# Kernel optimization log

Hardware: AMD Instinct MI355X
Metric: run time of the kernel (lower is better)

The kernel has to match this reference:

```python
import jax, jax.numpy as jnp
import numpy as np

def setup_inputs() -> dict:
    key = jax.random.key(0)
    k1, k2 = jax.random.split(key)
    bb_feats = jax.random.normal(k1, (8, 512, 128, 128), dtype=jnp.float32)
    aux_out = jax.random.normal(k2, (8, 19, 128, 128), dtype=jnp.float32)
    return {"bb_feats": bb_feats, "aux_out": aux_out}

def reference(bb_feats, aux_out):
    B, K, H, W = aux_out.shape
    C = bb_feats.shape[1]
    probs = jax.nn.softmax(aux_out.reshape(B, K, H * W), axis=2)  # [B,K,HW]
    feats = bb_feats.reshape(B, C, H * W)                          # [B,C,HW]
    # weighted sum over spatial dim: [B,K,HW] x [B,C,HW] -> [B,K,C]
    ctx = jnp.einsum('bks,bcs->bkc', probs, feats)
    # -> [B,C,K,1]
    return jnp.transpose(ctx, (0, 2, 1))[..., None]
```

## Files before the change

kernel.cpp:

```cpp
#include <hip/hip_runtime.h>
#include <math.h>

#define B 8
#define C 512
#define K 19
#define HW 16384
#define ROWS (B * K)
#define L2E 1.44269504088896340736f

#define NW 4
#define CPW 4
#define CPB (CPW * NW)
#define CG (C / CPB)
#define NSC 4
#define SCHUNK (HW / NSC)
#define TS 256
#define NT (SCHUNK / TS)

__global__ __launch_bounds__(1024)
void probs_kernel(const float* __restrict__ aux, float* __restrict__ probs,
                  float* __restrict__ out) {
    int row  = blockIdx.x;
    int tid  = threadIdx.x;
    int lane = tid & 63;
    int wave = tid >> 6;
    __shared__ float red[16];

    if (row < 19)
        ((float4*)out)[(size_t)row * 1024 + tid] = make_float4(0.f, 0.f, 0.f, 0.f);

    const float4* x4 = (const float4*)(aux + (size_t)row * HW);
    float4*       p4 = (float4*)(probs + (size_t)row * HW);

    float4 v[4];
    #pragma unroll
    for (int i = 0; i < 4; i++) v[i] = x4[tid + i * 1024];

    float m = -INFINITY;
    #pragma unroll
    for (int i = 0; i < 4; i++)
        m = fmaxf(m, fmaxf(fmaxf(v[i].x, v[i].y), fmaxf(v[i].z, v[i].w)));
    #pragma unroll
    for (int off = 32; off > 0; off >>= 1) m = fmaxf(m, __shfl_xor(m, off, 64));
    if (lane == 0) red[wave] = m;
    __syncthreads();
    #pragma unroll
    for (int w = 0; w < 16; w++) m = fmaxf(m, red[w]);
    __syncthreads();

    float nm = -m * L2E;
    float s = 0.f;
    #pragma unroll
    for (int i = 0; i < 4; i++) {
        v[i].x = exp2f(fmaf(v[i].x, L2E, nm));
        v[i].y = exp2f(fmaf(v[i].y, L2E, nm));
        v[i].z = exp2f(fmaf(v[i].z, L2E, nm));
        v[i].w = exp2f(fmaf(v[i].w, L2E, nm));
        s += (v[i].x + v[i].y) + (v[i].z + v[i].w);
    }
    #pragma unroll
    for (int off = 32; off > 0; off >>= 1) s += __shfl_xor(s, off, 64);
    if (lane == 0) red[wave] = s;
    __syncthreads();
    float Z = 0.f;
    #pragma unroll
    for (int w = 0; w < 16; w++) Z += red[w];
    float inv = 1.0f / Z;

    #pragma unroll
    for (int i = 0; i < 4; i++) {
        float4 o;
        o.x = v[i].x * inv; o.y = v[i].y * inv;
        o.z = v[i].z * inv; o.w = v[i].w * inv;
        p4[tid + i * 1024] = o;
    }
}

__global__ __launch_bounds__(256)
__attribute__((amdgpu_waves_per_eu(2)))
void gather_kernel(const float* __restrict__ feats, const float* __restrict__ probs,
                   float* __restrict__ out) {
    int bid = blockIdx.x;
    int xcd = bid & 7;
    int lid = xcd * 128 + (bid >> 3);
    int cg  = lid & (CG - 1);
    int grp = lid >> 5;
    int sc  = grp & (NSC - 1);
    int b   = grp >> 2;

    int tid  = threadIdx.x;
    int lane = tid & 63;
    int wave = tid >> 6;
    int c0   = cg * CPB + wave * CPW;

    const float* Pbase = probs + (size_t)b * K * HW + sc * SCHUNK + lane * 4;
    const float* Fbase = feats + ((size_t)b * C + c0) * HW + sc * SCHUNK;

    float acc[CPW][K];
    #pragma unroll
    for (int c = 0; c < CPW; c++)
        #pragma unroll
        for (int k = 0; k < K; k++) acc[c][k] = 0.f;

    float4 f_cur[CPW], f_next[CPW];
    #pragma unroll
    for (int c = 0; c < CPW; c++)
        f_cur[c] = *(const float4*)(Fbase + c * HW + lane * 4);

    for (int t = 0; t < NT; t++) {
        int s = t * TS;
        if (t + 1 < NT) {
            int s1 = s + TS;
            #pragma unroll
            for (int c = 0; c < CPW; c++)
                f_next[c] = *(const float4*)(Fbase + c * HW + s1 + lane * 4);
        }

        float4 p_cur = *(const float4*)(Pbase + s);
        #pragma unroll
        for (int k = 0; k < K; k++) {
            float4 p_nxt;
            if (k + 1 < K)
                p_nxt = *(const float4*)(Pbase + (size_t)(k + 1) * HW + s);
            #pragma unroll
            for (int c = 0; c < CPW; c++) {
                acc[c][k] = fmaf(p_cur.x, f_cur[c].x, acc[c][k]);
                acc[c][k] = fmaf(p_cur.y, f_cur[c].y, acc[c][k]);
                acc[c][k] = fmaf(p_cur.z, f_cur[c].z, acc[c][k]);
                acc[c][k] = fmaf(p_cur.w, f_cur[c].w, acc[c][k]);
            }
            p_cur = p_nxt;
        }

        #pragma unroll
        for (int c = 0; c < CPW; c++) f_cur[c] = f_next[c];
    }

    #pragma unroll
    for (int c = 0; c < CPW; c++)
        #pragma unroll
        for (int k = 0; k < K; k++) {
            float v = acc[c][k];
            #pragma unroll
            for (int off = 32; off > 0; off >>= 1) v += __shfl_xor(v, off, 64);
            if (lane == 0)
                atomicAdd(&out[((size_t)b * C + c0 + c) * K + k], v);
        }
}

extern "C" void kernel_launch(void* const* d_in, const int* in_sizes, int n_in,
                              void* d_out, int out_size, void* d_ws, size_t ws_size,
                              hipStream_t stream) {
    const float* feats = (const float*)d_in[0];
    const float* aux   = (const float*)d_in[1];
    float* out   = (float*)d_out;
    float* probs = (float*)d_ws;

    probs_kernel<<<ROWS, 1024, 0, stream>>>(aux, probs, out);
    gather_kernel<<<B * CG * NSC, 256, 0, stream>>>(feats, probs, out);
}
```

Measured before the change: 434.7 us.

## Stage probs tiles in LDS via async global_load_lds with double buffering

Each block now stages its shared probability tile (19 rows × 256 positions) into a double-buffered LDS array using async global_load_lds, instead of having every wave reload probs from global memory. Feature loads are double-buffered in registers, and manual vmcnt waits plus barriers order the pipeline. A per-block rotation of the tile order spreads concurrent blocks across different memory addresses. This is meant to cut redundant global and L2 traffic for probs and to overlap loads with FMAs, at the cost of block-wide barriers, extra LDS use, and fragile hand-counted waitcnt logic.

Result: faster. 399.8 us (-8.0%).

```diff
diff --git a/kernel.cpp b/kernel.cpp
--- a/kernel.cpp
+++ b/kernel.cpp
@@ -16,6 +16,9 @@
 #define SCHUNK (HW / NSC)
 #define TS 256
 #define NT (SCHUNK / TS)
+
+typedef __attribute__((address_space(3))) unsigned int lds_u32;
+typedef const __attribute__((address_space(1))) unsigned int glb_u32;
 
 __global__ __launch_bounds__(1024)
 void probs_kernel(const float* __restrict__ aux, float* __restrict__ probs,
@@ -80,6 +83,8 @@
 __attribute__((amdgpu_waves_per_eu(2)))
 void gather_kernel(const float* __restrict__ feats, const float* __restrict__ probs,
                    float* __restrict__ out) {
+    __shared__ float plds[2][K][TS];
+
     int bid = blockIdx.x;
     int xcd = bid & 7;
     int lid = xcd * 128 + (bid >> 3);
@@ -87,14 +92,15 @@
     int grp = lid >> 5;
     int sc  = grp & (NSC - 1);
     int b   = grp >> 2;
+    int rot = (bid * 11) & (NT - 1);
 
     int tid  = threadIdx.x;
     int lane = tid & 63;
     int wave = tid >> 6;
     int c0   = cg * CPB + wave * CPW;
 
-    const float* Pbase = probs + (size_t)b * K * HW + sc * SCHUNK + lane * 4;
-    const float* Fbase = feats + ((size_t)b * C + c0) * HW + sc * SCHUNK;
+    const float* Pbase = probs + (size_t)b * K * HW + sc * SCHUNK;
+    const float* Fbase = feats + ((size_t)b * C + c0) * HW + sc * SCHUNK + lane * 4;
 
     float acc[CPW][K];
     #pragma unroll
@@ -102,39 +108,57 @@
         #pragma unroll
         for (int k = 0; k < K; k++) acc[c][k] = 0.f;
 
-    float4 f_cur[CPW], f_next[CPW];
-    #pragma unroll
-    for (int c = 0; c < CPW; c++)
-        f_cur[c] = *(const float4*)(Fbase + c * HW + lane * 4);
+    float4 fA[CPW], fB[CPW];
 
-    for (int t = 0; t < NT; t++) {
-        int s = t * TS;
-        if (t + 1 < NT) {
-            int s1 = s + TS;
-            #pragma unroll
-            for (int c = 0; c < CPW; c++)
-                f_next[c] = *(const float4*)(Fbase + c * HW + s1 + lane * 4);
-        }
+#define SROT(t) ((((t) + rot) & (NT - 1)) * TS)
+#define STAGE(bi, t) do { int s_ = SROT(t); \
+    for (int k = wave; k < K; k += NW) \
+        __builtin_amdgcn_global_load_lds((glb_u32*)(Pbase + (size_t)k * HW + s_ + lane * 4), \
+                                         (lds_u32*)&plds[bi][k][0], 16, 0, 0); } while (0)
+#define FLOAD(fa, t) do { int s_ = SROT(t); \
+    _Pragma("unroll") for (int c = 0; c < CPW; c++) \
+        fa[c] = *(const float4*)(Fbase + (size_t)c * HW + s_); } while (0)
+#define FMATILE(bi, fa) do { \
+    _Pragma("unroll") for (int k = 0; k < K; k++) { \
+        float4 pv = *(const float4*)(&plds[bi][k][lane * 4]); \
+        _Pragma("unroll") for (int c = 0; c < CPW; c++) { \
+            acc[c][k] = fmaf(pv.x, fa[c].x, acc[c][k]); \
+            acc[c][k] = fmaf(pv.y, fa[c].y, acc[c][k]); \
+            acc[c][k] = fmaf(pv.z, fa[c].z, acc[c][k]); \
+            acc[c][k] = fmaf(pv.w, fa[c].w, acc[c][k]); } } } while (0)
+#define WAITB(keep) do { \
+    asm volatile("s_waitcnt vmcnt(" #keep ")" ::: "memory"); \
+    __builtin_amdgcn_sched_barrier(0); \
+    __builtin_amdgcn_s_barrier(); \
+    __builtin_amdgcn_sched_barrier(0); } while (0)
 
-        float4 p_cur = *(const float4*)(Pbase + s);
-        #pragma unroll
-        for (int k = 0; k < K; k++) {
-            float4 p_nxt;
-            if (k + 1 < K)
-                p_nxt = *(const float4*)(Pbase + (size_t)(k + 1) * HW + s);
-            #pragma unroll
-            for (int c = 0; c < CPW; c++) {
-                acc[c][k] = fmaf(p_cur.x, f_cur[c].x, acc[c][k]);
-                acc[c][k] = fmaf(p_cur.y, f_cur[c].y, acc[c][k]);
-                acc[c][k] = fmaf(p_cur.z, f_cur[c].z, acc[c][k]);
-                acc[c][k] = fmaf(p_cur.w, f_cur[c].w, acc[c][k]);
-            }
-            p_cur = p_nxt;
-        }
+    STAGE(0, 0);
+    FLOAD(fA, 0);
+    FLOAD(fB, 1);
 
-        #pragma unroll
-        for (int c = 0; c < CPW; c++) f_cur[c] = f_next[c];
+    #pragma unroll 1
+    for (int tp = 0; tp < 7; ++tp) {
+        int t = tp * 2;
+        WAITB(4);
+        STAGE(1, t + 1);
+        FMATILE(0, fA);
+        FLOAD(fA, t + 2);
+        WAITB(4);
+        STAGE(0, t + 2);
+        FMATILE(1, fB);
+        FLOAD(fB, t + 3);
     }
+    WAITB(4);
+    STAGE(1, 15);
+    FMATILE(0, fA);
+    WAITB(0);
+    FMATILE(1, fB);
+
+#undef SROT
+#undef STAGE
+#undef FLOAD
+#undef FMATILE
+#undef WAITB
 
     #pragma unroll
     for (int c = 0; c < CPW; c++)
```
